# Performance work log

Hardware: AMD Instinct MI355X
Metric: run time of the kernel (lower is better)

Reference implementation:

```python
import jax, jax.numpy as jnp
import numpy as np

B, IN, OUT = 512, 4096, 11008


def setup_inputs() -> dict:
    key = jax.random.key(0)
    k_x, k_stored, k_sign, k_scale, k_bias = jax.random.split(key, 5)
    x = jax.random.normal(k_x, (B, IN), dtype=jnp.float32)
    # QINS encoding: stored uint8 magnitude in [1, 255], sign in {-1, +1}
    stored = jax.random.randint(k_stored, (OUT, IN), 1, 256, dtype=jnp.int32)
    sign = 2 * jax.random.randint(k_sign, (OUT, IN), 0, 2, dtype=jnp.int32) - 1
    # log-range from from_linear's fallback calibration: weights in [e^-10, e^0]
    log_min = jnp.asarray(-10.0, dtype=jnp.float32)
    log_max = jnp.asarray(0.0, dtype=jnp.float32)
    # per-channel calibration scale, clamped to [0.5, 2.0] in from_linear
    scale = jax.random.uniform(k_scale, (OUT,), dtype=jnp.float32, minval=0.5, maxval=2.0)
    bias = jax.random.normal(k_bias, (OUT,), dtype=jnp.float32) * 0.01
    return {"x": x, "stored": stored, "sign": sign, "log_min": log_min,
            "log_max": log_max, "scale": scale, "bias": bias}


def reference(x, stored, sign, log_min, log_max, scale, bias):
    # Reconstruct fp32 weight from log-scale uint8 encoding (QINS)
    normalized = (255.0 - stored.astype(jnp.float32)) / 254.0      # [OUT, IN]
    log_w = log_min + normalized * (log_max - log_min)
    weight = sign.astype(jnp.float32) * jnp.exp(log_w)             # [OUT, IN]
    # y = (x @ W^T + b) * scale   (per-output-channel scale)
    out = jnp.einsum('bi,oi->bo', x, weight) + bias
    return out * scale
```

## Files before the change

kernel.cpp:

```cpp
#include <hip/hip_runtime.h>
#include <hip/hip_bf16.h>

#define B_DIM   512
#define IN_DIM  4096
#define OUT_DIM 11008

typedef __bf16 bf16x4 __attribute__((ext_vector_type(4)));
typedef __bf16 bf16x8 __attribute__((ext_vector_type(8)));
typedef float  floatx4 __attribute__((ext_vector_type(4)));

__global__ __launch_bounds__(256) void conv_x_kernel(
    const float* __restrict__ x, __bf16* __restrict__ xb) {
  int idx = blockIdx.x * blockDim.x + threadIdx.x;
  float4 v = ((const float4*)x)[idx];
  bf16x4 o;
  o[0] = (__bf16)v.x; o[1] = (__bf16)v.y; o[2] = (__bf16)v.z; o[3] = (__bf16)v.w;
  ((bf16x4*)xb)[idx] = o;
}

__device__ __forceinline__ void gl_lds16(const __bf16* g, __bf16* l) {
  __builtin_amdgcn_global_load_lds(
      (const __attribute__((address_space(1))) void*)g,
      (__attribute__((address_space(3))) void*)l, 16, 0, 0);
}

__device__ __forceinline__ void memfence_barrier() {
  asm volatile("" ::: "memory");
  __builtin_amdgcn_s_barrier();
  asm volatile("" ::: "memory");
}

__device__ __forceinline__ __bf16 dec1(int s, int g, float lmin, float slope) {
  return (__bf16)(__expf(lmin + (float)(255 - s) * slope) * (float)g);
}

__device__ __forceinline__ bf16x8 dec8(int4 sl, int4 sh, int4 gl, int4 gh,
                                       float lmin, float slope) {
  bf16x8 w;
  w[0] = dec1(sl.x, gl.x, lmin, slope);
  w[1] = dec1(sl.y, gl.y, lmin, slope);
  w[2] = dec1(sl.z, gl.z, lmin, slope);
  w[3] = dec1(sl.w, gl.w, lmin, slope);
  w[4] = dec1(sh.x, gh.x, lmin, slope);
  w[5] = dec1(sh.y, gh.y, lmin, slope);
  w[6] = dec1(sh.z, gh.z, lmin, slope);
  w[7] = dec1(sh.w, gh.w, lmin, slope);
  return w;
}

__global__ __launch_bounds__(256, 2) void fused_qins_gemm_kernel(
    const __bf16* __restrict__ A,
    const int* __restrict__ stored,
    const int* __restrict__ sign,
    const float* __restrict__ logmin, const float* __restrict__ logmax,
    const float* __restrict__ scale, const float* __restrict__ bias,
    float* __restrict__ out) {
  constexpr int K = IN_DIM, N = OUT_DIM;
  constexpr int BK = 32;
  constexpr int NIT = K / BK;
  constexpr int SBS = 40;

  __shared__ __align__(16) __bf16 sA[2][128 * BK];
  __shared__ __align__(16) __bf16 sB[64 * SBS];

  const int tid  = threadIdx.x;
  const int lane = tid & 63;
  const int wave = tid >> 6;
  const int wm   = (wave >> 1) * 64;
  const int wn   = (wave & 1) * 32;
  const int m16  = lane & 15;
  const int q    = lane >> 4;

  const int wg  = blockIdx.x;
  const int g   = (wg & 7) * 86 + (wg >> 3);
  const int bm0 = (g & 3) * 128;
  const int bn0 = (g >> 2) * 64;

  const float lmin  = logmin[0];
  const float slope = (logmax[0] - lmin) * (1.0f / 254.0f);

  const int rA   = tid >> 2;
  const int slot = (tid & 3) ^ (rA & 3);
  const __bf16* gA0 = A + (bm0 + rA) * K + slot * 8;
  const __bf16* gA1 = A + (bm0 + rA + 64) * K + slot * 8;
  const int aReadSlot = q ^ (m16 & 3);

  const int rB = tid >> 2;
  const int kq = (tid & 3) * 8;
  const int* pS = stored + (size_t)(bn0 + rB) * K + kq;
  const int* pG = sign   + (size_t)(bn0 + rB) * K + kq;
  __bf16* lB = sB + rB * SBS + kq;

  floatx4 acc[4][2] = {};

  int4 s0a = ((const int4*)pS)[0], s1a = ((const int4*)pS)[1];
  int4 g0a = ((const int4*)pG)[0], g1a = ((const int4*)pG)[1];
  int4 s0b = ((const int4*)(pS + BK))[0], s1b = ((const int4*)(pS + BK))[1];
  int4 g0b = ((const int4*)(pG + BK))[0], g1b = ((const int4*)(pG + BK))[1];
  gl_lds16(gA0, sA[0] + tid * 8);
  gl_lds16(gA1, sA[0] + 2048 + tid * 8);

#define BODY(i, S0, S1, G0, G1, CUR, NXT)                                     \
  {                                                                           \
    bf16x8 w = dec8(S0, S1, G0, G1, lmin, slope);                             \
    const int kt2 = ((i) + 2 < NIT) ? ((i) + 2) * BK : 0;                     \
    S0 = ((const int4*)(pS + kt2))[0]; S1 = ((const int4*)(pS + kt2))[1];     \
    G0 = ((const int4*)(pG + kt2))[0]; G1 = ((const int4*)(pG + kt2))[1];     \
    memfence_barrier();                   \
    *(bf16x8*)lB = w;                                                         \
    asm volatile("s_waitcnt vmcnt(4) lgkmcnt(0)" ::: "memory");               \
    const int kt1 = ((i) + 1 < NIT) ? ((i) + 1) * BK : 0;                     \
    gl_lds16(gA0 + kt1, (NXT) + tid * 8);                                     \
    gl_lds16(gA1 + kt1, (NXT) + 2048 + tid * 8);                              \
    memfence_barrier();                    \
    bf16x8 afr[4], bfr[2];                                                    \
    _Pragma("unroll")                                                         \
    for (int ii = 0; ii < 4; ++ii)                                            \
      afr[ii] = *(const bf16x8*)&(CUR)[(wm + ii * 16 + m16) * BK +            \
                                       aReadSlot * 8];                        \
    _Pragma("unroll")                                                         \
    for (int ii = 0; ii < 2; ++ii)                                            \
      bfr[ii] = *(const bf16x8*)&sB[(wn + ii * 16 + m16) * SBS + q * 8];      \
    _Pragma("unroll")                                                         \
    for (int mi = 0; mi < 4; ++mi)                                            \
      _Pragma("unroll")                                                       \
      for (int ni = 0; ni < 2; ++ni)                                          \
        acc[mi][ni] = __builtin_amdgcn_mfma_f32_16x16x32_bf16(                \
            afr[mi], bfr[ni], acc[mi][ni], 0, 0, 0);                          \
  }

  for (int it = 0; it < NIT; it += 2) {
    BODY(it,     s0a, s1a, g0a, g1a, sA[0], sA[1]);
    BODY(it + 1, s0b, s1b, g0b, g1b, sA[1], sA[0]);
  }
#undef BODY

#pragma unroll
  for (int ni = 0; ni < 2; ++ni) {
    const int col = bn0 + wn + ni * 16 + m16;
    const float sc = scale[col];
    const float bb = bias[col] * sc;
#pragma unroll
    for (int mi = 0; mi < 4; ++mi) {
#pragma unroll
      for (int r = 0; r < 4; ++r) {
        const int row = bm0 + wm + mi * 16 + q * 4 + r;
        out[row * N + col] = acc[mi][ni][r] * sc + bb;
      }
    }
  }
}

extern "C" void kernel_launch(void* const* d_in, const int* in_sizes, int n_in,
                              void* d_out, int out_size, void* d_ws, size_t ws_size,
                              hipStream_t stream) {
  const float* x      = (const float*)d_in[0];
  const int*   stored = (const int*)d_in[1];
  const int*   sign   = (const int*)d_in[2];
  const float* logmin = (const float*)d_in[3];
  const float* logmax = (const float*)d_in[4];
  const float* scale  = (const float*)d_in[5];
  const float* bias   = (const float*)d_in[6];
  float* out = (float*)d_out;

  __bf16* wsX = (__bf16*)d_ws;

  conv_x_kernel<<<2048, 256, 0, stream>>>(x, wsX);
  fused_qins_gemm_kernel<<<688, 256, 0, stream>>>(
      wsX, stored, sign, logmin, logmax, scale, bias, out);
}
```

Before: 461.9 us.

## Double-buffer decoded weight tile and use a single barrier per K-step

Double-buffers the decoded B tile in LDS, dropping the padded layout in favour of an XOR swizzle shared with the A tile. Each K-step now uses one barrier instead of two. Weight decode for the next tile runs after the current fragments are read from LDS, with sched_barriers to pin instruction order. The stored/sign prefetch distance grows to three tiles, which keeps more registers live and adds a prologue decode.

```diff
diff --git a/kernel.cpp b/kernel.cpp
--- a/kernel.cpp
+++ b/kernel.cpp
@@ -22,12 +22,6 @@
   __builtin_amdgcn_global_load_lds(
       (const __attribute__((address_space(1))) void*)g,
       (__attribute__((address_space(3))) void*)l, 16, 0, 0);
-}
-
-__device__ __forceinline__ void memfence_barrier() {
-  asm volatile("" ::: "memory");
-  __builtin_amdgcn_s_barrier();
-  asm volatile("" ::: "memory");
 }
 
 __device__ __forceinline__ __bf16 dec1(int s, int g, float lmin, float slope) {
@@ -58,10 +52,9 @@
   constexpr int K = IN_DIM, N = OUT_DIM;
   constexpr int BK = 32;
   constexpr int NIT = K / BK;
-  constexpr int SBS = 40;
 
   __shared__ __align__(16) __bf16 sA[2][128 * BK];
-  __shared__ __align__(16) __bf16 sB[64 * SBS];
+  __shared__ __align__(16) __bf16 sB[2][64 * BK];
 
   const int tid  = threadIdx.x;
   const int lane = tid & 63;
@@ -79,48 +72,67 @@
   const float lmin  = logmin[0];
   const float slope = (logmax[0] - lmin) * (1.0f / 254.0f);
 
-  const int rA   = tid >> 2;
-  const int slot = (tid & 3) ^ (rA & 3);
-  const __bf16* gA0 = A + (bm0 + rA) * K + slot * 8;
-  const __bf16* gA1 = A + (bm0 + rA + 64) * K + slot * 8;
-  const int aReadSlot = q ^ (m16 & 3);
+  const int rS = tid >> 2;
+  const int cS = tid & 3;
+  const int fS = (rS ^ (rS >> 2)) & 3;
+  const int wSlot = cS ^ fS;
+  const int rdSlot = q ^ ((m16 ^ (m16 >> 2)) & 3);
 
-  const int rB = tid >> 2;
-  const int kq = (tid & 3) * 8;
-  const int* pS = stored + (size_t)(bn0 + rB) * K + kq;
-  const int* pG = sign   + (size_t)(bn0 + rB) * K + kq;
-  __bf16* lB = sB + rB * SBS + kq;
+  const __bf16* gA0 = A + (size_t)(bm0 + rS) * K + wSlot * 8;
+  const __bf16* gA1 = A + (size_t)(bm0 + rS + 64) * K + wSlot * 8;
+
+  const int* pS = stored + (size_t)(bn0 + rS) * K + cS * 8;
+  const int* pG = sign   + (size_t)(bn0 + rS) * K + cS * 8;
+  const int wOff = rS * BK + wSlot * 8;
 
   floatx4 acc[4][2] = {};
 
-  int4 s0a = ((const int4*)pS)[0], s1a = ((const int4*)pS)[1];
-  int4 g0a = ((const int4*)pG)[0], g1a = ((const int4*)pG)[1];
-  int4 s0b = ((const int4*)(pS + BK))[0], s1b = ((const int4*)(pS + BK))[1];
-  int4 g0b = ((const int4*)(pG + BK))[0], g1b = ((const int4*)(pG + BK))[1];
-  gl_lds16(gA0, sA[0] + tid * 8);
-  gl_lds16(gA1, sA[0] + 2048 + tid * 8);
+  {
+    int4 ps0 = ((const int4*)pS)[0], ps1 = ((const int4*)pS)[1];
+    int4 pg0 = ((const int4*)pG)[0], pg1 = ((const int4*)pG)[1];
+    bf16x8 w = dec8(ps0, ps1, pg0, pg1, lmin, slope);
+    *(bf16x8*)&sB[0][wOff] = w;
+  }
+  gl_lds16(gA0, &sA[0][tid * 8]);
+  gl_lds16(gA1, &sA[0][2048 + tid * 8]);
+  int4 s0a = ((const int4*)(pS + BK))[0],     s1a = ((const int4*)(pS + BK))[1];
+  int4 g0a = ((const int4*)(pG + BK))[0],     g1a = ((const int4*)(pG + BK))[1];
+  int4 s0b = ((const int4*)(pS + 2 * BK))[0], s1b = ((const int4*)(pS + 2 * BK))[1];
+  int4 g0b = ((const int4*)(pG + 2 * BK))[0], g1b = ((const int4*)(pG + 2 * BK))[1];
+  asm volatile("s_waitcnt vmcnt(0) lgkmcnt(0)" ::: "memory");
 
-#define BODY(i, S0, S1, G0, G1, CUR, NXT)                                     \
+#define STEP(T, CUR, NXT, S0, S1, G0, G1)                                     \
   {                                                                           \
-    bf16x8 w = dec8(S0, S1, G0, G1, lmin, slope);                             \
-    const int kt2 = ((i) + 2 < NIT) ? ((i) + 2) * BK : 0;                     \
-    S0 = ((const int4*)(pS + kt2))[0]; S1 = ((const int4*)(pS + kt2))[1];     \
-    G0 = ((const int4*)(pG + kt2))[0]; G1 = ((const int4*)(pG + kt2))[1];     \
-    memfence_barrier();                   \
-    *(bf16x8*)lB = w;                                                         \
-    asm volatile("s_waitcnt vmcnt(4) lgkmcnt(0)" ::: "memory");               \
-    const int kt1 = ((i) + 1 < NIT) ? ((i) + 1) * BK : 0;                     \
-    gl_lds16(gA0 + kt1, (NXT) + tid * 8);                                     \
-    gl_lds16(gA1 + kt1, (NXT) + 2048 + tid * 8);                              \
-    memfence_barrier();                    \
+    asm volatile("s_waitcnt vmcnt(4)" ::: "memory");                          \
+    __builtin_amdgcn_s_barrier();                                             \
+    __builtin_amdgcn_sched_barrier(0);                                        \
     bf16x8 afr[4], bfr[2];                                                    \
     _Pragma("unroll")                                                         \
     for (int ii = 0; ii < 4; ++ii)                                            \
-      afr[ii] = *(const bf16x8*)&(CUR)[(wm + ii * 16 + m16) * BK +            \
-                                       aReadSlot * 8];                        \
+      afr[ii] = *(const bf16x8*)&sA[CUR][(wm + ii * 16 + m16) * BK +          \
+                                         rdSlot * 8];                         \
     _Pragma("unroll")                                                         \
     for (int ii = 0; ii < 2; ++ii)                                            \
-      bfr[ii] = *(const bf16x8*)&sB[(wn + ii * 16 + m16) * SBS + q * 8];      \
+      bfr[ii] = *(const bf16x8*)&sB[CUR][(wn + ii * 16 + m16) * BK +          \
+                                         rdSlot * 8];                         \
+    bf16x8 w = dec8(S0, S1, G0, G1, lmin, slope);                             \
+    *(bf16x8*)&sB[NXT][wOff] = w;                                             \
+    __builtin_amdgcn_sched_barrier(0);                                        \
+    {                                                                         \
+      const int ktA = ((T) + 1 < NIT) ? ((T) + 1) * BK : 0;                   \
+      gl_lds16(gA0 + ktA, &sA[NXT][tid * 8]);                                 \
+      gl_lds16(gA1 + ktA, &sA[NXT][2048 + tid * 8]);                          \
+    }                                                                         \
+    __builtin_amdgcn_sched_barrier(0);                                        \
+    {                                                                         \
+      const int ktB = ((T) + 3 < NIT) ? ((T) + 3) * BK : 0;                   \
+      S0 = ((const int4*)(pS + ktB))[0];                                      \
+      S1 = ((const int4*)(pS + ktB))[1];                                      \
+      G0 = ((const int4*)(pG + ktB))[0];                                      \
+      G1 = ((const int4*)(pG + ktB))[1];                                      \
+    }                                                                         \
+    asm volatile("s_waitcnt lgkmcnt(0)" ::: "memory");                        \
+    __builtin_amdgcn_sched_barrier(0);                                        \
     _Pragma("unroll")                                                         \
     for (int mi = 0; mi < 4; ++mi)                                            \
       _Pragma("unroll")                                                       \
@@ -129,11 +141,11 @@
             afr[mi], bfr[ni], acc[mi][ni], 0, 0, 0);                          \
   }
 
-  for (int it = 0; it < NIT; it += 2) {
-    BODY(it,     s0a, s1a, g0a, g1a, sA[0], sA[1]);
-    BODY(it + 1, s0b, s1b, g0b, g1b, sA[1], sA[0]);
+  for (int t = 0; t < NIT; t += 2) {
+    STEP(t,     0, 1, s0a, s1a, g0a, g1a);
+    STEP(t + 1, 1, 0, s0b, s1b, g0b, g1b);
   }
-#undef BODY
+#undef STEP
 
 #pragma unroll
   for (int ni = 0; ni < 2; ++ni) {
```

New measurement: 477.1 us. +3.3%, slower.

## Decode weights directly into MFMA registers, dropping the B LDS staging

Applied to the files above, without the earlier changes.

Each wave now loads the stored/sign ints for its own B fragment and decodes them straight into the bf16 MFMA operand registers, removing the shared-memory B tile, its store, and one barrier per K step. Decoding uses an fma plus a sign-bit XOR instead of a float multiply. Occupancy is raised to 3 workgroups per CU and the A LDS swizzle is removed. The trade-off is that the two waves sharing each n-column half now decode the same weights twice, adding global load traffic and exp work. Dropping the swizzle may also introduce LDS bank conflicts on A reads.

```diff
diff --git a/kernel.cpp b/kernel.cpp
--- a/kernel.cpp
+++ b/kernel.cpp
@@ -24,31 +24,26 @@
       (__attribute__((address_space(3))) void*)l, 16, 0, 0);
 }
 
-__device__ __forceinline__ void memfence_barrier() {
-  asm volatile("" ::: "memory");
-  __builtin_amdgcn_s_barrier();
-  asm volatile("" ::: "memory");
-}
-
-__device__ __forceinline__ __bf16 dec1(int s, int g, float lmin, float slope) {
-  return (__bf16)(__expf(lmin + (float)(255 - s) * slope) * (float)g);
+__device__ __forceinline__ float dec1f(int s, int g, float lmin, float slope) {
+  float e = __expf(fmaf((float)(255 - s), slope, lmin));
+  return __uint_as_float(__float_as_uint(e) ^ ((unsigned)g & 0x80000000u));
 }
 
 __device__ __forceinline__ bf16x8 dec8(int4 sl, int4 sh, int4 gl, int4 gh,
                                        float lmin, float slope) {
   bf16x8 w;
-  w[0] = dec1(sl.x, gl.x, lmin, slope);
-  w[1] = dec1(sl.y, gl.y, lmin, slope);
-  w[2] = dec1(sl.z, gl.z, lmin, slope);
-  w[3] = dec1(sl.w, gl.w, lmin, slope);
-  w[4] = dec1(sh.x, gh.x, lmin, slope);
-  w[5] = dec1(sh.y, gh.y, lmin, slope);
-  w[6] = dec1(sh.z, gh.z, lmin, slope);
-  w[7] = dec1(sh.w, gh.w, lmin, slope);
+  w[0] = (__bf16)dec1f(sl.x, gl.x, lmin, slope);
+  w[1] = (__bf16)dec1f(sl.y, gl.y, lmin, slope);
+  w[2] = (__bf16)dec1f(sl.z, gl.z, lmin, slope);
+  w[3] = (__bf16)dec1f(sl.w, gl.w, lmin, slope);
+  w[4] = (__bf16)dec1f(sh.x, gh.x, lmin, slope);
+  w[5] = (__bf16)dec1f(sh.y, gh.y, lmin, slope);
+  w[6] = (__bf16)dec1f(sh.z, gh.z, lmin, slope);
+  w[7] = (__bf16)dec1f(sh.w, gh.w, lmin, slope);
   return w;
 }
 
-__global__ __launch_bounds__(256, 2) void fused_qins_gemm_kernel(
+__global__ __launch_bounds__(256, 3) void fused_qins_gemm_kernel(
     const __bf16* __restrict__ A,
     const int* __restrict__ stored,
     const int* __restrict__ sign,
@@ -58,10 +53,8 @@
   constexpr int K = IN_DIM, N = OUT_DIM;
   constexpr int BK = 32;
   constexpr int NIT = K / BK;
-  constexpr int SBS = 40;
 
   __shared__ __align__(16) __bf16 sA[2][128 * BK];
-  __shared__ __align__(16) __bf16 sB[64 * SBS];
 
   const int tid  = threadIdx.x;
   const int lane = tid & 63;
@@ -79,59 +72,60 @@
   const float lmin  = logmin[0];
   const float slope = (logmax[0] - lmin) * (1.0f / 254.0f);
 
-  const int rA   = tid >> 2;
-  const int slot = (tid & 3) ^ (rA & 3);
-  const __bf16* gA0 = A + (bm0 + rA) * K + slot * 8;
-  const __bf16* gA1 = A + (bm0 + rA + 64) * K + slot * 8;
-  const int aReadSlot = q ^ (m16 & 3);
+  const int r0 = tid >> 2;
+  const int c0 = (tid & 3) * 8;
+  const __bf16* gA0 = A + (size_t)(bm0 + r0) * K + c0;
+  const __bf16* gA1 = A + (size_t)(bm0 + r0 + 64) * K + c0;
 
-  const int rB = tid >> 2;
-  const int kq = (tid & 3) * 8;
-  const int* pS = stored + (size_t)(bn0 + rB) * K + kq;
-  const int* pG = sign   + (size_t)(bn0 + rB) * K + kq;
-  __bf16* lB = sB + rB * SBS + kq;
+  const int rB0 = bn0 + wn + m16;
+  const int* bS0 = stored + (size_t)rB0 * K + q * 8;
+  const int* bS1 = bS0 + 16 * K;
+  const int* bG0 = sign + (size_t)rB0 * K + q * 8;
+  const int* bG1 = bG0 + 16 * K;
 
   floatx4 acc[4][2] = {};
 
-  int4 s0a = ((const int4*)pS)[0], s1a = ((const int4*)pS)[1];
-  int4 g0a = ((const int4*)pG)[0], g1a = ((const int4*)pG)[1];
-  int4 s0b = ((const int4*)(pS + BK))[0], s1b = ((const int4*)(pS + BK))[1];
-  int4 g0b = ((const int4*)(pG + BK))[0], g1b = ((const int4*)(pG + BK))[1];
-  gl_lds16(gA0, sA[0] + tid * 8);
-  gl_lds16(gA1, sA[0] + 2048 + tid * 8);
+  gl_lds16(gA0, &sA[0][tid * 8]);
+  gl_lds16(gA1, &sA[0][2048 + tid * 8]);
+  int4 as0 = *(const int4*)(bS0),     as1 = *(const int4*)(bS0 + 4);
+  int4 as2 = *(const int4*)(bS1),     as3 = *(const int4*)(bS1 + 4);
+  int4 ag0 = *(const int4*)(bG0),     ag1 = *(const int4*)(bG0 + 4);
+  int4 ag2 = *(const int4*)(bG1),     ag3 = *(const int4*)(bG1 + 4);
+  int4 bs0, bs1, bs2, bs3, bg0, bg1, bg2, bg3;
 
-#define BODY(i, S0, S1, G0, G1, CUR, NXT)                                     \
+#define BODY(T, CUR, NXT, S0, S1, S2, S3, G0, G1, G2, G3,                     \
+             T0, T1, T2, T3, U0, U1, U2, U3)                                  \
   {                                                                           \
-    bf16x8 w = dec8(S0, S1, G0, G1, lmin, slope);                             \
-    const int kt2 = ((i) + 2 < NIT) ? ((i) + 2) * BK : 0;                     \
-    S0 = ((const int4*)(pS + kt2))[0]; S1 = ((const int4*)(pS + kt2))[1];     \
-    G0 = ((const int4*)(pG + kt2))[0]; G1 = ((const int4*)(pG + kt2))[1];     \
-    memfence_barrier();                   \
-    *(bf16x8*)lB = w;                                                         \
-    asm volatile("s_waitcnt vmcnt(4) lgkmcnt(0)" ::: "memory");               \
-    const int kt1 = ((i) + 1 < NIT) ? ((i) + 1) * BK : 0;                     \
-    gl_lds16(gA0 + kt1, (NXT) + tid * 8);                                     \
-    gl_lds16(gA1 + kt1, (NXT) + 2048 + tid * 8);                              \
-    memfence_barrier();                    \
-    bf16x8 afr[4], bfr[2];                                                    \
+    __syncthreads();                                                          \
+    const int ktn = ((T) + 1 < NIT) ? ((T) + 1) * BK : 0;                     \
+    if ((T) + 1 < NIT) {                                                      \
+      gl_lds16(gA0 + ktn, &sA[NXT][tid * 8]);                                 \
+      gl_lds16(gA1 + ktn, &sA[NXT][2048 + tid * 8]);                          \
+    }                                                                         \
+    bf16x8 afr[4];                                                            \
     _Pragma("unroll")                                                         \
     for (int ii = 0; ii < 4; ++ii)                                            \
-      afr[ii] = *(const bf16x8*)&(CUR)[(wm + ii * 16 + m16) * BK +            \
-                                       aReadSlot * 8];                        \
+      afr[ii] = *(const bf16x8*)&sA[CUR][(wm + ii * 16 + m16) * BK + q * 8];  \
+    T0 = *(const int4*)(bS0 + ktn); T1 = *(const int4*)(bS0 + ktn + 4);       \
+    T2 = *(const int4*)(bS1 + ktn); T3 = *(const int4*)(bS1 + ktn + 4);       \
+    U0 = *(const int4*)(bG0 + ktn); U1 = *(const int4*)(bG0 + ktn + 4);       \
+    U2 = *(const int4*)(bG1 + ktn); U3 = *(const int4*)(bG1 + ktn + 4);       \
+    bf16x8 bfr0 = dec8(S0, S1, G0, G1, lmin, slope);                          \
+    bf16x8 bfr1 = dec8(S2, S3, G2, G3, lmin, slope);                          \
     _Pragma("unroll")                                                         \
-    for (int ii = 0; ii < 2; ++ii)                                            \
-      bfr[ii] = *(const bf16x8*)&sB[(wn + ii * 16 + m16) * SBS + q * 8];      \
-    _Pragma("unroll")                                                         \
-    for (int mi = 0; mi < 4; ++mi)                                            \
-      _Pragma("unroll")                                                       \
-      for (int ni = 0; ni < 2; ++ni)                                          \
-        acc[mi][ni] = __builtin_amdgcn_mfma_f32_16x16x32_bf16(                \
-            afr[mi], bfr[ni], acc[mi][ni], 0, 0, 0);                          \
+    for (int mi = 0; mi < 4; ++mi) {                                          \
+      acc[mi][0] = __builtin_amdgcn_mfma_f32_16x16x32_bf16(                   \
+          afr[mi], bfr0, acc[mi][0], 0, 0, 0);                                \
+      acc[mi][1] = __builtin_amdgcn_mfma_f32_16x16x32_bf16(                   \
+          afr[mi], bfr1, acc[mi][1], 0, 0, 0);                                \
+    }                                                                         \
   }
 
-  for (int it = 0; it < NIT; it += 2) {
-    BODY(it,     s0a, s1a, g0a, g1a, sA[0], sA[1]);
-    BODY(it + 1, s0b, s1b, g0b, g1b, sA[1], sA[0]);
+  for (int t = 0; t < NIT; t += 2) {
+    BODY(t,     0, 1, as0, as1, as2, as3, ag0, ag1, ag2, ag3,
+                      bs0, bs1, bs2, bs3, bg0, bg1, bg2, bg3);
+    BODY(t + 1, 1, 0, bs0, bs1, bs2, bs3, bg0, bg1, bg2, bg3,
+                      as0, as1, as2, as3, ag0, ag1, ag2, ag3);
   }
 #undef BODY
 
```

Result: slower. 932.9 us (+102.0%).
